# Kernel tuning notes

Measured on AMD Instinct MI355X. Metric: run time of the kernel, lower is better.

The kernel has to match this reference:

```python
import jax, jax.numpy as jnp
import numpy as np

B, T, N, C, H = 4, 64, 2048, 32, 64
SLOPE = 0.2


def setup_inputs() -> dict:
    key = jax.random.key(0)
    ks = jax.random.split(key, 8)
    x = jax.random.normal(ks[0], (B, T, N, C), dtype=jnp.float32)
    # GRU params (single layer), torch gate order: r, z, n
    s_ih = 1.0 / np.sqrt(H)
    w_ih = jax.random.uniform(ks[1], (3 * H, C), jnp.float32, -s_ih, s_ih)
    w_hh = jax.random.uniform(ks[2], (3 * H, H), jnp.float32, -s_ih, s_ih)
    b_ih = jax.random.uniform(ks[3], (3 * H,), jnp.float32, -s_ih, s_ih)
    b_hh = jax.random.uniform(ks[4], (3 * H,), jnp.float32, -s_ih, s_ih)
    # xavier_uniform for (H,1) projections: bound = sqrt(6/(H+1))
    bnd = float(np.sqrt(6.0 / (H + 1)))
    wk = jax.random.uniform(ks[5], (H, 1), jnp.float32, -bnd, bnd)
    wq = jax.random.uniform(ks[6], (H, 1), jnp.float32, -bnd, bnd)
    return {"x": x, "w_ih": w_ih, "w_hh": w_hh, "b_ih": b_ih, "b_hh": b_hh,
            "wk": wk, "wq": wq}


def _gru_last_hidden(xs, w_ih, w_hh, b_ih, b_hh):
    # xs: [T, M, C] -> final hidden [M, H]
    M = xs.shape[1]
    h0 = jnp.zeros((M, H), dtype=xs.dtype)

    def step(h, xt):
        gi = xt @ w_ih.T + b_ih          # [M, 3H]
        gh = h @ w_hh.T + b_hh           # [M, 3H]
        i_r, i_z, i_n = jnp.split(gi, 3, axis=-1)
        h_r, h_z, h_n = jnp.split(gh, 3, axis=-1)
        r = jax.nn.sigmoid(i_r + h_r)
        z = jax.nn.sigmoid(i_z + h_z)
        n = jnp.tanh(i_n + r * h_n)
        h_new = (1.0 - z) * n + z * h
        return h_new, None

    h_last, _ = jax.lax.scan(step, h0, xs)
    return h_last


def reference(x, w_ih, w_hh, b_ih, b_hh, wk, wq):
    b, t, n, c = x.shape
    # [B,T,N,C] -> [T, B*N, C]
    xs = jnp.transpose(x, (1, 0, 2, 3)).reshape(t, b * n, c)
    h_last = _gru_last_hidden(xs, w_ih, w_hh, b_ih, b_hh)  # [B*N, H]
    node_embed = h_last.reshape(b, n, H)
    key = node_embed @ wk                       # [B, N, 1]
    query = node_embed @ wq                     # [B, N, 1]
    scores = key + jnp.swapaxes(query, 1, 2)    # [B, N, N]
    scores = jnp.where(scores >= 0, scores, SLOPE * scores)
    attn = jax.nn.softmax(scores, axis=-1)      # dropout p=0 (eval)
    adj = attn.mean(axis=0)                     # [N, N]
    adj = 0.5 * (adj + adj.T)                   # symmetric=True
    return adj
```

## Files before the change

### kernel.cpp

```cpp
#include <hip/hip_runtime.h>
#include <math.h>

#define B_ 4
#define T_ 64
#define N_ 2048
#define C_ 32
#define H_ 64
#define M_ (B_*N_)
#define SLOPE 0.2f
#define LOG2E 1.44269504088896340736f

typedef __attribute__((ext_vector_type(8))) _Float16 half8;
typedef __attribute__((ext_vector_type(4))) float floatx4;

#define MFMA16H(a,b,c) __builtin_amdgcn_mfma_f32_16x16x32_f16(a,b,c,0,0,0)

#define BARRIER() asm volatile("s_waitcnt lgkmcnt(0)\n\ts_barrier" ::: "memory")

__device__ __forceinline__ float lrelu(float v) { return fmaxf(v, SLOPE * v); }
__device__ __forceinline__ float frcp(float x)  { return __builtin_amdgcn_rcpf(x); }
__device__ __forceinline__ float fexp2(float x) { float r; asm("v_exp_f32 %0, %1" : "=v"(r) : "v"(x)); return r; }

__device__ __forceinline__ half8 cvt8h(float4 a, float4 b) {
    half8 h;
    h[0]=(_Float16)a.x; h[1]=(_Float16)a.y; h[2]=(_Float16)a.z; h[3]=(_Float16)a.w;
    h[4]=(_Float16)b.x; h[5]=(_Float16)b.y; h[6]=(_Float16)b.z; h[7]=(_Float16)b.w;
    return h;
}
__device__ __forceinline__ half8 cvt8s(const float* f, float sc) {
    half8 h;
    #pragma unroll
    for (int e = 0; e < 8; ++e) h[e] = (_Float16)(f[e] * sc);
    return h;
}

__global__ __launch_bounds__(256, 2) void gru_kernel(
    const float* __restrict__ x,
    const float* __restrict__ w_ih,
    const float* __restrict__ w_hh,
    const float* __restrict__ b_ih,
    const float* __restrict__ b_hh,
    const float* __restrict__ wk_p,
    const float* __restrict__ wq_p,
    float* __restrict__ key,
    float* __restrict__ query)
{
    __shared__ __align__(16) _Float16 hh[2][16][64];
    __shared__ float kq_lds[2][16][4];

    const int tid   = threadIdx.x;
    const int lane  = tid & 63;
    const int w     = tid >> 6;
    const int col16 = lane & 15;
    const int kgrp  = lane >> 4;

    const int m0 = blockIdx.x * 16;
    const int b  = m0 >> 11;
    const int n0 = m0 & 2047;

    const float gsc[3] = {-LOG2E, LOG2E, 2.f*LOG2E};

    half8 whhF[3][2];
    half8 wihF[3];
    #pragma unroll
    for (int g = 0; g < 3; ++g) {
        const int rw = g*64 + w*16 + col16;
        #pragma unroll
        for (int kb = 0; kb < 2; ++kb)
            whhF[g][kb] = cvt8s(w_hh + rw*64 + kb*32 + kgrp*8, gsc[g]);
        wihF[g] = cvt8s(w_ih + rw*32 + kgrp*8, gsc[g]);
    }
    const int jcol = w*16 + col16;
    const float br  = -LOG2E     * (b_ih[jcol]    + b_hh[jcol]);
    const float bz  =  LOG2E     * (b_ih[64+jcol] + b_hh[64+jcol]);
    const float bin =  2.f*LOG2E * b_ih[128+jcol];
    const float bhn =  2.f*LOG2E * b_hh[128+jcol];
    const floatx4 bR4  = {br, br, br, br};
    const floatx4 bZ4  = {bz, bz, bz, bz};
    const floatx4 bNI4 = {bin, bin, bin, bin};
    const floatx4 bNH4 = {bhn, bhn, bhn, bhn};

    const float wkj = wk_p[jcol] * LOG2E;
    const float wqj = wq_p[jcol] * LOG2E;

    const float* xlane = x + ((size_t)b*T_*N_ + (n0 + col16))*C_ + kgrp*8;
    const int xstride = N_*C_;

    for (int idx = tid; idx < 16*64/2; idx += 256)
        ((int*)&hh[0][0][0])[idx] = 0;

    floatx4 xR, xZ, xNI;
    {
        const half8 ax = cvt8h(*(const float4*)xlane, *(const float4*)(xlane + 4));
        xR  = MFMA16H(ax, wihF[0], bR4);
        xZ  = MFMA16H(ax, wihF[1], bZ4);
        xNI = MFMA16H(ax, wihF[2], bNI4);
    }
    float4 pAa = *(const float4*)(xlane + xstride);
    float4 pAb = *(const float4*)(xlane + xstride + 4);
    float4 pBa = {0,0,0,0}, pBb = {0,0,0,0};
    BARRIER();

    float hp[4] = {0.f, 0.f, 0.f, 0.f};

#define GRU_STEP(T, CUR, FXa, FXb, GXa, GXb) do {                               \
    const int nxt_ = (CUR) ^ 1;                                                 \
    half8 ah[2];                                                                \
    _Pragma("unroll")                                                           \
    for (int kb = 0; kb < 2; ++kb) {                                            \
        const int ke = (kgrp*8 + kb*32) ^ ((col16 >> 2) << 4);                  \
        ah[kb] = *(const half8*)&hh[CUR][col16][ke];                            \
    }                                                                           \
      \
    __builtin_amdgcn_s_setprio(1);                                              \
    floatx4 aR  = MFMA16H(ah[0], whhF[0][0], xR);                               \
    floatx4 aZ  = MFMA16H(ah[0], whhF[1][0], xZ);                               \
    floatx4 aNH = MFMA16H(ah[0], whhF[2][0], bNH4);                             \
    aR  = MFMA16H(ah[1], whhF[0][1], aR);                                       \
    aZ  = MFMA16H(ah[1], whhF[1][1], aZ);                                       \
    aNH = MFMA16H(ah[1], whhF[2][1], aNH);                                      \
    __builtin_amdgcn_s_setprio(0);                                              \
                 \
    _Pragma("unroll")                                                           \
    for (int s = 0; s < 4; ++s) {                                               \
        const float tr = frcp(1.f + fexp2(aR[s]));                   \
        const float v  = fmaf(tr, aNH[s], xNI[s]);                              \
        const float tn = frcp(1.f + fexp2(v));                                  \
        const float nn = fmaf(tn, -2.f, 1.f);                         \
        const float tw = frcp(1.f + fexp2(aZ[s]));                   \
        const float h  = fmaf(tw, nn - hp[s], hp[s]);                           \
        hp[s] = h;                                                              \
        const int r = kgrp*4 + s;                                               \
        const int c = jcol ^ (kgrp << 4);                                       \
        hh[nxt_][r][c] = (_Float16)h;                                           \
    }                                                                           \
         \
    if ((T) + 1 < T_) {                                                         \
        const half8 ax = cvt8h(FXa, FXb);                                       \
        xR  = MFMA16H(ax, wihF[0], bR4);                                        \
        xZ  = MFMA16H(ax, wihF[1], bZ4);                                        \
        xNI = MFMA16H(ax, wihF[2], bNI4);                                       \
    }                                                                           \
    if ((T) + 2 < T_) {                                  \
        GXa = *(const float4*)(xlane + (size_t)((T)+2) * xstride);              \
        GXb = *(const float4*)(xlane + (size_t)((T)+2) * xstride + 4);          \
    }                                                                           \
    BARRIER();                                                                  \
} while (0)

    for (int t = 0; t < T_; t += 2) {
        GRU_STEP(t,     0, pAa, pAb, pBa, pBb);
        GRU_STEP(t + 1, 1, pBa, pBb, pAa, pAb);
    }
#undef GRU_STEP

    float kp[4], qp[4];
    #pragma unroll
    for (int s = 0; s < 4; ++s) { kp[s] = hp[s] * wkj; qp[s] = hp[s] * wqj; }
    #pragma unroll
    for (int mask = 8; mask; mask >>= 1) {
        #pragma unroll
        for (int s = 0; s < 4; ++s) {
            kp[s] += __shfl_xor(kp[s], mask);
            qp[s] += __shfl_xor(qp[s], mask);
        }
    }
    if (col16 == 0) {
        #pragma unroll
        for (int s = 0; s < 4; ++s) {
            kq_lds[0][kgrp*4 + s][w] = kp[s];
            kq_lds[1][kgrp*4 + s][w] = qp[s];
        }
    }
    __syncthreads();
    if (tid < 32) {
        const int smp = tid & 15, sel = tid >> 4;
        const float v = kq_lds[sel][smp][0] + kq_lds[sel][smp][1]
                      + kq_lds[sel][smp][2] + kq_lds[sel][smp][3];
        (sel ? query : key)[m0 + smp] = v;
    }
}

__global__ __launch_bounds__(256) void den_kernel(
    const float* __restrict__ key, const float* __restrict__ query,
    float* __restrict__ den)
{
    int idx  = (blockIdx.x * 256 + threadIdx.x) >> 6;
    int lane = threadIdx.x & 63;
    int b    = idx >> 11;
    float ki = key[idx];
    const float4* q4 = (const float4*)(query + ((size_t)b << 11));
    float sum = 0.f;
    for (int jj = lane; jj < N_/4; jj += 64) {
        float4 qv = q4[jj];
        sum += fexp2(lrelu(ki + qv.x)) + fexp2(lrelu(ki + qv.y))
             + fexp2(lrelu(ki + qv.z)) + fexp2(lrelu(ki + qv.w));
    }
    #pragma unroll
    for (int off = 32; off; off >>= 1) sum += __shfl_down(sum, off);
    if (lane == 0) den[idx] = frcp(sum);
}

__global__ __launch_bounds__(256) void out_kernel(
    const float* __restrict__ key, const float* __restrict__ query,
    const float* __restrict__ den, float* __restrict__ out)
{
    const int flat = blockIdx.x * 256 + threadIdx.x;
    const int i  = flat >> 9;
    const int j0 = (flat & 511) << 2;
    float4 acc = {0.f, 0.f, 0.f, 0.f};
    #pragma unroll
    for (int b = 0; b < B_; ++b) {
        const int bi = (b << 11) + i, bj = (b << 11) + j0;
        const float ki = key[bi], qi = query[bi], di = den[bi];
        const float4 k4 = *(const float4*)&key[bj];
        const float4 q4 = *(const float4*)&query[bj];
        const float4 d4 = *(const float4*)&den[bj];
        acc.x = fmaf(fexp2(lrelu(ki + q4.x)), di, acc.x);
        acc.y = fmaf(fexp2(lrelu(ki + q4.y)), di, acc.y);
        acc.z = fmaf(fexp2(lrelu(ki + q4.z)), di, acc.z);
        acc.w = fmaf(fexp2(lrelu(ki + q4.w)), di, acc.w);
        acc.x = fmaf(fexp2(lrelu(k4.x + qi)), d4.x, acc.x);
        acc.y = fmaf(fexp2(lrelu(k4.y + qi)), d4.y, acc.y);
        acc.z = fmaf(fexp2(lrelu(k4.z + qi)), d4.z, acc.z);
        acc.w = fmaf(fexp2(lrelu(k4.w + qi)), d4.w, acc.w);
    }
    acc.x *= 0.125f; acc.y *= 0.125f; acc.z *= 0.125f; acc.w *= 0.125f;
    ((float4*)out)[flat] = acc;
}

extern "C" void kernel_launch(void* const* d_in, const int* in_sizes, int n_in,
                              void* d_out, int out_size, void* d_ws, size_t ws_size,
                              hipStream_t stream) {
    const float* x    = (const float*)d_in[0];
    const float* w_ih = (const float*)d_in[1];
    const float* w_hh = (const float*)d_in[2];
    const float* b_ih = (const float*)d_in[3];
    const float* b_hh = (const float*)d_in[4];
    const float* wk   = (const float*)d_in[5];
    const float* wq   = (const float*)d_in[6];
    float* out = (float*)d_out;
    float* ws  = (float*)d_ws;

    float* key   = ws;
    float* query = ws + 8192;
    float* den   = ws + 16384;

    gru_kernel<<<M_/16, 256, 0, stream>>>(x, w_ih, w_hh, b_ih, b_hh,
                                          wk, wq, key, query);
    den_kernel<<<M_/4, 256, 0, stream>>>(key, query, den);
    out_kernel<<<(N_*N_/4)/256, 256, 0, stream>>>(key, query, den, out);
}
```

Measured before the change: 69.04 us.

## Run each GRU tile in a single wavefront to drop per-step block barriers

The GRU recurrence for a 16-row tile now runs in one 64-lane wavefront that computes all four 16-column hidden slices itself, instead of four waves sharing the work. The per-timestep s_barrier becomes a plain LDS wait, and the key/query reduction goes straight to global memory without the shared-memory cross-wave step. The next step's input-projection MFMAs are also split around the gate math so they can overlap with it. In exchange each wave holds four times the weight fragments and accumulators in registers and issues four times the MFMAs per step, which raises register pressure and serializes work that used to be spread across waves.

```diff
diff --git a/kernel.cpp b/kernel.cpp
--- a/kernel.cpp
+++ b/kernel.cpp
@@ -15,7 +15,7 @@
 
 #define MFMA16H(a,b,c) __builtin_amdgcn_mfma_f32_16x16x32_f16(a,b,c,0,0,0)
 
-#define BARRIER() asm volatile("s_waitcnt lgkmcnt(0)\n\ts_barrier" ::: "memory")
+#define FENCE() asm volatile("s_waitcnt lgkmcnt(0)" ::: "memory")
 
 __device__ __forceinline__ float lrelu(float v) { return fmaxf(v, SLOPE * v); }
 __device__ __forceinline__ float frcp(float x)  { return __builtin_amdgcn_rcpf(x); }
@@ -34,7 +34,7 @@
     return h;
 }
 
-__global__ __launch_bounds__(256, 2) void gru_kernel(
+__global__ __launch_bounds__(64, 1) void gru_kernel(
     const float* __restrict__ x,
     const float* __restrict__ w_ih,
     const float* __restrict__ w_hh,
@@ -46,13 +46,10 @@
     float* __restrict__ query)
 {
     __shared__ __align__(16) _Float16 hh[2][16][64];
-    __shared__ float kq_lds[2][16][4];
-
-    const int tid   = threadIdx.x;
-    const int lane  = tid & 63;
-    const int w     = tid >> 6;
-    const int col16 = lane & 15;
-    const int kgrp  = lane >> 4;
+
+    const int lane = threadIdx.x;
+    const int c  = lane & 15;
+    const int kg = lane >> 4;
 
     const int m0 = blockIdx.x * 16;
     const int b  = m0 >> 11;
@@ -60,92 +57,123 @@
 
     const float gsc[3] = {-LOG2E, LOG2E, 2.f*LOG2E};
 
-    half8 whhF[3][2];
-    half8 wihF[3];
-    #pragma unroll
-    for (int g = 0; g < 3; ++g) {
-        const int rw = g*64 + w*16 + col16;
-        #pragma unroll
-        for (int kb = 0; kb < 2; ++kb)
-            whhF[g][kb] = cvt8s(w_hh + rw*64 + kb*32 + kgrp*8, gsc[g]);
-        wihF[g] = cvt8s(w_ih + rw*32 + kgrp*8, gsc[g]);
-    }
-    const int jcol = w*16 + col16;
-    const float br  = -LOG2E     * (b_ih[jcol]    + b_hh[jcol]);
-    const float bz  =  LOG2E     * (b_ih[64+jcol] + b_hh[64+jcol]);
-    const float bin =  2.f*LOG2E * b_ih[128+jcol];
-    const float bhn =  2.f*LOG2E * b_hh[128+jcol];
-    const floatx4 bR4  = {br, br, br, br};
-    const floatx4 bZ4  = {bz, bz, bz, bz};
-    const floatx4 bNI4 = {bin, bin, bin, bin};
-    const floatx4 bNH4 = {bhn, bhn, bhn, bhn};
-
-    const float wkj = wk_p[jcol] * LOG2E;
-    const float wqj = wq_p[jcol] * LOG2E;
-
-    const float* xlane = x + ((size_t)b*T_*N_ + (n0 + col16))*C_ + kgrp*8;
+    half8 whhF[3][2][4];
+    half8 wihF[3][4];
+    #pragma unroll
+    for (int gt = 0; gt < 3; ++gt)
+        #pragma unroll
+        for (int n = 0; n < 4; ++n) {
+            const int rw = gt*64 + n*16 + c;
+            #pragma unroll
+            for (int kb = 0; kb < 2; ++kb)
+                whhF[gt][kb][n] = cvt8s(w_hh + rw*64 + kb*32 + kg*8, gsc[gt]);
+            wihF[gt][n] = cvt8s(w_ih + rw*32 + kg*8, gsc[gt]);
+        }
+
+    floatx4 bR4[4], bZ4[4], bNI4[4], bNH4[4];
+    float wkj[4], wqj[4];
+    #pragma unroll
+    for (int n = 0; n < 4; ++n) {
+        const int j = n*16 + c;
+        const float br  = -LOG2E     * (b_ih[j]    + b_hh[j]);
+        const float bz  =  LOG2E     * (b_ih[64+j] + b_hh[64+j]);
+        const float bin =  2.f*LOG2E * b_ih[128+j];
+        const float bhn =  2.f*LOG2E * b_hh[128+j];
+        bR4[n]  = (floatx4){br, br, br, br};
+        bZ4[n]  = (floatx4){bz, bz, bz, bz};
+        bNI4[n] = (floatx4){bin, bin, bin, bin};
+        bNH4[n] = (floatx4){bhn, bhn, bhn, bhn};
+        wkj[n] = wk_p[j] * LOG2E;
+        wqj[n] = wq_p[j] * LOG2E;
+    }
+
+    const float* xlane = x + ((size_t)b*T_*N_ + (n0 + c))*C_ + kg*8;
     const int xstride = N_*C_;
 
-    for (int idx = tid; idx < 16*64/2; idx += 256)
-        ((int*)&hh[0][0][0])[idx] = 0;
-
-    floatx4 xR, xZ, xNI;
+    #pragma unroll
+    for (int i = 0; i < 8; ++i)
+        ((int*)&hh[0][0][0])[lane + i*64] = 0;
+
+    floatx4 xR[4], xZ[4], xNI[4];
     {
         const half8 ax = cvt8h(*(const float4*)xlane, *(const float4*)(xlane + 4));
-        xR  = MFMA16H(ax, wihF[0], bR4);
-        xZ  = MFMA16H(ax, wihF[1], bZ4);
-        xNI = MFMA16H(ax, wihF[2], bNI4);
+        #pragma unroll
+        for (int n = 0; n < 4; ++n) {
+            xR[n]  = MFMA16H(ax, wihF[0][n], bR4[n]);
+            xZ[n]  = MFMA16H(ax, wihF[1][n], bZ4[n]);
+            xNI[n] = MFMA16H(ax, wihF[2][n], bNI4[n]);
+        }
     }
     float4 pAa = *(const float4*)(xlane + xstride);
     float4 pAb = *(const float4*)(xlane + xstride + 4);
     float4 pBa = {0,0,0,0}, pBb = {0,0,0,0};
-    BARRIER();
-
-    float hp[4] = {0.f, 0.f, 0.f, 0.f};
+    FENCE();
+
+    float hp[4][4];
+    #pragma unroll
+    for (int n = 0; n < 4; ++n)
+        #pragma unroll
+        for (int s = 0; s < 4; ++s) hp[n][s] = 0.f;
 
 #define GRU_STEP(T, CUR, FXa, FXb, GXa, GXb) do {                               \
     const int nxt_ = (CUR) ^ 1;                                                 \
     half8 ah[2];                                                                \
     _Pragma("unroll")                                                           \
     for (int kb = 0; kb < 2; ++kb) {                                            \
-        const int ke = (kgrp*8 + kb*32) ^ ((col16 >> 2) << 4);                  \
-        ah[kb] = *(const half8*)&hh[CUR][col16][ke];                            \
-    }                                                                           \
-      \
-    __builtin_amdgcn_s_setprio(1);                                              \
-    floatx4 aR  = MFMA16H(ah[0], whhF[0][0], xR);                               \
-    floatx4 aZ  = MFMA16H(ah[0], whhF[1][0], xZ);                               \
-    floatx4 aNH = MFMA16H(ah[0], whhF[2][0], bNH4);                             \
-    aR  = MFMA16H(ah[1], whhF[0][1], aR);                                       \
-    aZ  = MFMA16H(ah[1], whhF[1][1], aZ);                                       \
-    aNH = MFMA16H(ah[1], whhF[2][1], aNH);                                      \
-    __builtin_amdgcn_s_setprio(0);                                              \
-                 \
-    _Pragma("unroll")                                                           \
-    for (int s = 0; s < 4; ++s) {                                               \
-        const float tr = frcp(1.f + fexp2(aR[s]));                   \
-        const float v  = fmaf(tr, aNH[s], xNI[s]);                              \
-        const float tn = frcp(1.f + fexp2(v));                                  \
-        const float nn = fmaf(tn, -2.f, 1.f);                         \
-        const float tw = frcp(1.f + fexp2(aZ[s]));                   \
-        const float h  = fmaf(tw, nn - hp[s], hp[s]);                           \
-        hp[s] = h;                                                              \
-        const int r = kgrp*4 + s;                                               \
-        const int c = jcol ^ (kgrp << 4);                                       \
-        hh[nxt_][r][c] = (_Float16)h;                                           \
-    }                                                                           \
-         \
+        const int ke = (kg*8 + kb*32) ^ ((c >> 2) << 4);                        \
+        ah[kb] = *(const half8*)&hh[CUR][c][ke];                                \
+    }                                                                           \
+                  \
+    floatx4 aR[4], aZ[4], aNH[4];                                               \
+    _Pragma("unroll")                                                           \
+    for (int n = 0; n < 4; ++n) {                                               \
+        aR[n]  = MFMA16H(ah[0], whhF[0][0][n], xR[n]);                          \
+        aZ[n]  = MFMA16H(ah[0], whhF[1][0][n], xZ[n]);                          \
+        aNH[n] = MFMA16H(ah[0], whhF[2][0][n], bNH4[n]);                        \
+    }                                                                           \
+    _Pragma("unroll")                                                           \
+    for (int n = 0; n < 4; ++n) {                                               \
+        aR[n]  = MFMA16H(ah[1], whhF[0][1][n], aR[n]);                          \
+        aZ[n]  = MFMA16H(ah[1], whhF[1][1][n], aZ[n]);                          \
+        aNH[n] = MFMA16H(ah[1], whhF[2][1][n], aNH[n]);                         \
+    }                                                                           \
+                \
+    half8 ax_;                                                                  \
     if ((T) + 1 < T_) {                                                         \
-        const half8 ax = cvt8h(FXa, FXb);                                       \
-        xR  = MFMA16H(ax, wihF[0], bR4);                                        \
-        xZ  = MFMA16H(ax, wihF[1], bZ4);                                        \
-        xNI = MFMA16H(ax, wihF[2], bNI4);                                       \
+        ax_ = cvt8h(FXa, FXb);                                                  \
+        _Pragma("unroll")                                                       \
+        for (int n = 0; n < 4; ++n) {                                           \
+            xR[n] = MFMA16H(ax_, wihF[0][n], bR4[n]);                           \
+            xZ[n] = MFMA16H(ax_, wihF[1][n], bZ4[n]);                           \
+        }                                                                       \
     }                                                                           \
     if ((T) + 2 < T_) {                                  \
         GXa = *(const float4*)(xlane + (size_t)((T)+2) * xstride);              \
         GXb = *(const float4*)(xlane + (size_t)((T)+2) * xstride + 4);          \
     }                                                                           \
-    BARRIER();                                                                  \
+                 \
+    _Pragma("unroll")                                                           \
+    for (int n = 0; n < 4; ++n) {                                               \
+        _Pragma("unroll")                                                       \
+        for (int s = 0; s < 4; ++s) {                                           \
+            const float tr = frcp(1.f + fexp2(aR[n][s]));            \
+            const float v  = fmaf(tr, aNH[n][s], xNI[n][s]);                    \
+            const float tn = frcp(1.f + fexp2(v));                              \
+            const float nn = fmaf(tn, -2.f, 1.f);                     \
+            const float tw = frcp(1.f + fexp2(aZ[n][s]));            \
+            const float h  = fmaf(tw, nn - hp[n][s], hp[n][s]);                 \
+            hp[n][s] = h;                                                       \
+            const int m = kg*4 + s;                                             \
+            hh[nxt_][m][(n ^ kg)*16 + c] = (_Float16)h;      \
+        }                                                                       \
+    }                                                                           \
+            \
+    if ((T) + 1 < T_) {                                                         \
+        _Pragma("unroll")                                                       \
+        for (int n = 0; n < 4; ++n)                                             \
+            xNI[n] = MFMA16H(ax_, wihF[2][n], bNI4[n]);                         \
+    }                                                                           \
+    FENCE();                                                                    \
 } while (0)
 
     for (int t = 0; t < T_; t += 2) {
@@ -156,7 +184,15 @@
 
     float kp[4], qp[4];
     #pragma unroll
-    for (int s = 0; s < 4; ++s) { kp[s] = hp[s] * wkj; qp[s] = hp[s] * wqj; }
+    for (int s = 0; s < 4; ++s) {
+        float kv = 0.f, qv = 0.f;
+        #pragma unroll
+        for (int n = 0; n < 4; ++n) {
+            kv = fmaf(hp[n][s], wkj[n], kv);
+            qv = fmaf(hp[n][s], wqj[n], qv);
+        }
+        kp[s] = kv; qp[s] = qv;
+    }
     #pragma unroll
     for (int mask = 8; mask; mask >>= 1) {
         #pragma unroll
@@ -165,19 +201,12 @@
             qp[s] += __shfl_xor(qp[s], mask);
         }
     }
-    if (col16 == 0) {
+    if (c == 0) {
         #pragma unroll
         for (int s = 0; s < 4; ++s) {
-            kq_lds[0][kgrp*4 + s][w] = kp[s];
-            kq_lds[1][kgrp*4 + s][w] = qp[s];
-        }
-    }
-    __syncthreads();
-    if (tid < 32) {
-        const int smp = tid & 15, sel = tid >> 4;
-        const float v = kq_lds[sel][smp][0] + kq_lds[sel][smp][1]
-                      + kq_lds[sel][smp][2] + kq_lds[sel][smp][3];
-        (sel ? query : key)[m0 + smp] = v;
+            key  [m0 + kg*4 + s] = kp[s];
+            query[m0 + kg*4 + s] = qp[s];
+        }
     }
 }
 
@@ -246,8 +275,8 @@
     float* query = ws + 8192;
     float* den   = ws + 16384;
 
-    gru_kernel<<<M_/16, 256, 0, stream>>>(x, w_ih, w_hh, b_ih, b_hh,
-                                          wk, wq, key, query);
+    gru_kernel<<<M_/16, 64, 0, stream>>>(x, w_ih, w_hh, b_ih, b_hh,
+                                         wk, wq, key, query);
     den_kernel<<<M_/4, 256, 0, stream>>>(key, query, den);
     out_kernel<<<(N_*N_/4)/256, 256, 0, stream>>>(key, query, den, out);
 }
```

Measured after the change: 105.4 us. +52.7%, slower.
